# Optimization experiments

Measured on AMD Instinct MI355X. Metric: run time of the kernel, lower is better.

The kernel has to match this reference:

```python
import jax, jax.numpy as jnp
import numpy as np

HIDDEN = 32

def setup_inputs() -> dict:
    key = jax.random.key(0)
    ks = jax.random.split(key, 7)
    B, T = 131072, 128
    return {
        "x": jax.random.normal(ks[0], (B, T, 1), dtype=jnp.float32),
        "W_ih": jax.random.normal(ks[1], (4 * HIDDEN, 1), dtype=jnp.float32) * 0.1,
        "W_hh": jax.random.normal(ks[2], (4 * HIDDEN, HIDDEN), dtype=jnp.float32) * 0.1,
        "b_ih": jax.random.normal(ks[3], (4 * HIDDEN,), dtype=jnp.float32) * 0.1,
        "b_hh": jax.random.normal(ks[4], (4 * HIDDEN,), dtype=jnp.float32) * 0.1,
        "W_fc": jax.random.normal(ks[5], (2, HIDDEN), dtype=jnp.float32) * 0.1,
        "b_fc": jax.random.normal(ks[6], (2,), dtype=jnp.float32) * 0.1,
    }

def _lstm_scan(x, W_ih, W_hh, b_ih, b_hh):
    B = x.shape[0]
    h0 = jnp.zeros((B, HIDDEN), dtype=x.dtype)
    c0 = jnp.zeros((B, HIDDEN), dtype=x.dtype)
    xs = jnp.swapaxes(x, 0, 1)  # [T, B, 1]

    def step(carry, xt):
        h, c = carry
        # gates: [B, 4H]; PyTorch LSTMCell gate order: i, f, g, o
        gates = xt @ W_ih.T + b_ih + h @ W_hh.T + b_hh
        i, f, g, o = jnp.split(gates, 4, axis=-1)
        c_new = jax.nn.sigmoid(f) * c + jax.nn.sigmoid(i) * jnp.tanh(g)
        h_new = jax.nn.sigmoid(o) * jnp.tanh(c_new)
        return (h_new, c_new), None

    (h, _), _ = jax.lax.scan(step, (h0, c0), xs)
    return h

def reference(x, W_ih, W_hh, b_ih, b_hh, W_fc, b_fc):
    h = _lstm_scan(x, W_ih, W_hh, b_ih, b_hh)
    return h @ W_fc.T + b_fc  # [B, 2]
```

## Files before the change

### kernel.cpp

```cpp
#include <hip/hip_runtime.h>
#include <hip/hip_bf16.h>

#define T_STEPS 128
#define L2E  1.44269504f
#define L2E2 2.88539008f

typedef __attribute__((ext_vector_type(8))) short short8;
typedef __attribute__((ext_vector_type(4))) float f32x4;

extern "C" __global__ void __launch_bounds__(256)
lstm_mfma_kernel(const float* __restrict__ x,
                 const float* __restrict__ W_ih,
                 const float* __restrict__ W_hh,
                 const float* __restrict__ b_ih,
                 const float* __restrict__ b_hh,
                 const float* __restrict__ W_fc,
                 const float* __restrict__ b_fc,
                 float* __restrict__ out, int B)
{
    __shared__ unsigned int hhi[4][256];
    __shared__ unsigned int hlo[4][256];

    const int widx = threadIdx.x >> 6;
    const int lane = threadIdx.x & 63;
    const int p    = lane & 15;
    const int g4   = lane >> 4;
    const int btile = (blockIdx.x * 4 + widx) * 16;
    if (btile >= B) return;

    unsigned int* hh = &hhi[widx][0];
    unsigned int* hl = &hlo[widx][0];

    #pragma unroll
    for (int q = 0; q < 4; ++q) { hh[q * 64 + lane] = 0u; hl[q * 64 + lane] = 0u; }

    short8 wfrag[8];
    float  biasv[8], wihv[8];
    #pragma unroll
    for (int m = 0; m < 8; ++m) {
        int gu = (m >> 1) * 32 + 2 * p + (m & 1);
        float scale = (m >> 1) == 2 ? L2E2 : L2E;
        biasv[m] = (b_ih[gu] + b_hh[gu]) * scale;
        wihv[m]  = W_ih[gu] * scale;
        const float* wr = W_hh + gu * 32 + g4 * 8;
        short8 w;
        #pragma unroll
        for (int e = 0; e < 8; ++e) {
            unsigned int bits = __float_as_uint(wr[e] * scale);
            bits = bits + 0x7FFFu + ((bits >> 16) & 1u);
            w[e] = (short)(bits >> 16);
        }
        wfrag[m] = w;
    }

    __builtin_amdgcn_wave_barrier();

    const float* xrow = x + (size_t)(btile + g4 * 4) * T_STEPS;

    float cst[2][4];
    float hn[2][4];
    #pragma unroll
    for (int u = 0; u < 2; ++u)
        #pragma unroll
        for (int r = 0; r < 4; ++r) cst[u][r] = 0.0f;

    for (int tb = 0; tb < T_STEPS; tb += 4) {
        f32x4 xq[4];
        #pragma unroll
        for (int r = 0; r < 4; ++r)
            xq[r] = *reinterpret_cast<const f32x4*>(xrow + r * T_STEPS + tb);

        #pragma unroll
        for (int s = 0; s < 4; ++s) {
            f32x4 acc[8];
            #pragma unroll
            for (int m = 0; m < 8; ++m) {
                f32x4 a;
                #pragma unroll
                for (int r = 0; r < 4; ++r) a[r] = fmaf(xq[r][s], wihv[m], biasv[m]);
                acc[m] = a;
            }

            short8 ahi = *reinterpret_cast<short8*>(&hh[p * 16 + g4 * 4]);
            short8 alo = *reinterpret_cast<short8*>(&hl[p * 16 + g4 * 4]);

            #pragma unroll
            for (int m = 0; m < 8; ++m) {
                acc[m] = __builtin_amdgcn_mfma_f32_16x16x32_bf16(ahi, wfrag[m], acc[m], 0, 0, 0);
                acc[m] = __builtin_amdgcn_mfma_f32_16x16x32_bf16(alo, wfrag[m], acc[m], 0, 0, 0);
            }

            #pragma unroll
            for (int u = 0; u < 2; ++u) {
                #pragma unroll
                for (int r = 0; r < 4; ++r) {
                    float ei = __builtin_amdgcn_exp2f(acc[0 + u][r]);
                    float ef = __builtin_amdgcn_exp2f(acc[2 + u][r]);
                    float eg = __builtin_amdgcn_exp2f(acc[4 + u][r]);
                    float eo = __builtin_amdgcn_exp2f(acc[6 + u][r]);
                    float ef1 = ef + 1.0f, ei1 = ei + 1.0f, eg1 = eg + 1.0f;
                    float P   = ei1 * eg1;
                    float num = fmaf(ef * cst[u][r], P, ei * (eg - 1.0f) * ef1);
                    float cn  = num * __builtin_amdgcn_rcpf(P * ef1);
                    cst[u][r] = cn;
                    float ec  = __builtin_amdgcn_exp2f(cn * L2E2);
                    hn[u][r]  = eo * (ec - 1.0f)
                              * __builtin_amdgcn_rcpf((eo + 1.0f) * (ec + 1.0f));
                }
            }

            #pragma unroll
            for (int r = 0; r < 4; ++r) {
                unsigned int x0 = __float_as_uint(hn[0][r]);
                unsigned int x1 = __float_as_uint(hn[1][r]);
                unsigned int hiw = (x0 >> 16) | (x1 & 0xFFFF0000u);
                float res0 = hn[0][r] - __uint_as_float(x0 & 0xFFFF0000u);
                float res1 = hn[1][r] - __uint_as_float(x1 & 0xFFFF0000u);
                unsigned int low = (__float_as_uint(res0) >> 16)
                                 | (__float_as_uint(res1) & 0xFFFF0000u);
                int rb = g4 * 4 + r;
                hh[rb * 16 + p] = hiw;
                hl[rb * 16 + p] = low;
            }
            __builtin_amdgcn_wave_barrier();
        }
    }

    float wfc00 = W_fc[2 * p], wfc01 = W_fc[2 * p + 1];
    float wfc10 = W_fc[32 + 2 * p], wfc11 = W_fc[32 + 2 * p + 1];
    float bfc0 = b_fc[0], bfc1 = b_fc[1];
    #pragma unroll
    for (int r = 0; r < 4; ++r) {
        float o0 = fmaf(hn[0][r], wfc00, hn[1][r] * wfc01);
        float o1 = fmaf(hn[0][r], wfc10, hn[1][r] * wfc11);
        #pragma unroll
        for (int m = 8; m >= 1; m >>= 1) {
            o0 += __shfl_xor(o0, m, 64);
            o1 += __shfl_xor(o1, m, 64);
        }
        if (p == 0) {
            size_t b = (size_t)(btile + g4 * 4 + r);
            out[b * 2 + 0] = o0 + bfc0;
            out[b * 2 + 1] = o1 + bfc1;
        }
    }
}

extern "C" void kernel_launch(void* const* d_in, const int* in_sizes, int n_in,
                              void* d_out, int out_size, void* d_ws, size_t ws_size,
                              hipStream_t stream) {
    const float* x    = (const float*)d_in[0];
    const float* W_ih = (const float*)d_in[1];
    const float* W_hh = (const float*)d_in[2];
    const float* b_ih = (const float*)d_in[3];
    const float* b_hh = (const float*)d_in[4];
    const float* W_fc = (const float*)d_in[5];
    const float* b_fc = (const float*)d_in[6];
    float* out = (float*)d_out;

    int B = in_sizes[0] / T_STEPS;
    int grid = (B + 63) / 64;
    hipLaunchKernelGGL(lstm_mfma_kernel, dim3(grid), dim3(256), 0, stream,
                       x, W_ih, W_hh, b_ih, b_hh, W_fc, b_fc, out, B);
}
```

Before: 747.5 us.

## Batch reciprocals across lanes, swizzle LDS layout, and pack h with v_perm

Vectorizes the per-step LSTM cell math over f32x4 and replaces per-element reciprocals with shared ones. One rcp now serves four cell denominators and one rcp serves each pair of h denominators, using product tricks, which cuts transcendental instructions per step. The LDS write and read addresses are swizzled (pp permutation, rows written as 4*R+g4) to change the bank pattern, and bf16 hi/lo packing now uses v_perm. Batching the reciprocals adds multiplies and risks overflow or precision loss when the products of denominators grow large.

```diff
diff --git a/kernel.cpp b/kernel.cpp
--- a/kernel.cpp
+++ b/kernel.cpp
@@ -57,12 +57,12 @@
 
     const float* xrow = x + (size_t)(btile + g4 * 4) * T_STEPS;
 
-    float cst[2][4];
-    float hn[2][4];
-    #pragma unroll
-    for (int u = 0; u < 2; ++u)
-        #pragma unroll
-        for (int r = 0; r < 4; ++r) cst[u][r] = 0.0f;
+    const int pp = ((p & 3) << 2) | (p >> 2);
+    const int rdoff = pp * 16 + g4 * 4;
+
+    f32x4 cst4[2];
+    f32x4 hn4[2];
+    cst4[0] = 0.0f; cst4[1] = 0.0f;
 
     for (int tb = 0; tb < T_STEPS; tb += 4) {
         f32x4 xq[4];
@@ -72,17 +72,16 @@
 
         #pragma unroll
         for (int s = 0; s < 4; ++s) {
+            f32x4 xs;
+            xs[0] = xq[0][s]; xs[1] = xq[1][s]; xs[2] = xq[2][s]; xs[3] = xq[3][s];
+
             f32x4 acc[8];
             #pragma unroll
-            for (int m = 0; m < 8; ++m) {
-                f32x4 a;
-                #pragma unroll
-                for (int r = 0; r < 4; ++r) a[r] = fmaf(xq[r][s], wihv[m], biasv[m]);
-                acc[m] = a;
-            }
-
-            short8 ahi = *reinterpret_cast<short8*>(&hh[p * 16 + g4 * 4]);
-            short8 alo = *reinterpret_cast<short8*>(&hl[p * 16 + g4 * 4]);
+            for (int m = 0; m < 8; ++m)
+                acc[m] = xs * wihv[m] + biasv[m];
+
+            short8 ahi = *reinterpret_cast<short8*>(&hh[rdoff]);
+            short8 alo = *reinterpret_cast<short8*>(&hl[rdoff]);
 
             #pragma unroll
             for (int m = 0; m < 8; ++m) {
@@ -90,38 +89,87 @@
                 acc[m] = __builtin_amdgcn_mfma_f32_16x16x32_bf16(alo, wfrag[m], acc[m], 0, 0, 0);
             }
 
-            #pragma unroll
-            for (int u = 0; u < 2; ++u) {
-                #pragma unroll
-                for (int r = 0; r < 4; ++r) {
-                    float ei = __builtin_amdgcn_exp2f(acc[0 + u][r]);
-                    float ef = __builtin_amdgcn_exp2f(acc[2 + u][r]);
-                    float eg = __builtin_amdgcn_exp2f(acc[4 + u][r]);
-                    float eo = __builtin_amdgcn_exp2f(acc[6 + u][r]);
-                    float ef1 = ef + 1.0f, ei1 = ei + 1.0f, eg1 = eg + 1.0f;
-                    float P   = ei1 * eg1;
-                    float num = fmaf(ef * cst[u][r], P, ei * (eg - 1.0f) * ef1);
-                    float cn  = num * __builtin_amdgcn_rcpf(P * ef1);
-                    cst[u][r] = cn;
-                    float ec  = __builtin_amdgcn_exp2f(cn * L2E2);
-                    hn[u][r]  = eo * (ec - 1.0f)
-                              * __builtin_amdgcn_rcpf((eo + 1.0f) * (ec + 1.0f));
-                }
-            }
-
-            #pragma unroll
-            for (int r = 0; r < 4; ++r) {
-                unsigned int x0 = __float_as_uint(hn[0][r]);
-                unsigned int x1 = __float_as_uint(hn[1][r]);
-                unsigned int hiw = (x0 >> 16) | (x1 & 0xFFFF0000u);
-                float res0 = hn[0][r] - __uint_as_float(x0 & 0xFFFF0000u);
-                float res1 = hn[1][r] - __uint_as_float(x1 & 0xFFFF0000u);
-                unsigned int low = (__float_as_uint(res0) >> 16)
-                                 | (__float_as_uint(res1) & 0xFFFF0000u);
-                int rb = g4 * 4 + r;
-                hh[rb * 16 + p] = hiw;
-                hl[rb * 16 + p] = low;
-            }
+            #define CELL4(U) {                                                  \
+                f32x4 gi = acc[0 + (U)];                                        \
+                f32x4 gf = acc[2 + (U)];                                        \
+                f32x4 gg = acc[4 + (U)];                                        \
+                f32x4 go = acc[6 + (U)];                                        \
+                f32x4 ei, ef, eg, eo;                                           \
+                ei[0] = __builtin_amdgcn_exp2f(gi[0]);                          \
+                ei[1] = __builtin_amdgcn_exp2f(gi[1]);                          \
+                ei[2] = __builtin_amdgcn_exp2f(gi[2]);                          \
+                ei[3] = __builtin_amdgcn_exp2f(gi[3]);                          \
+                ef[0] = __builtin_amdgcn_exp2f(gf[0]);                          \
+                ef[1] = __builtin_amdgcn_exp2f(gf[1]);                          \
+                ef[2] = __builtin_amdgcn_exp2f(gf[2]);                          \
+                ef[3] = __builtin_amdgcn_exp2f(gf[3]);                          \
+                eg[0] = __builtin_amdgcn_exp2f(gg[0]);                          \
+                eg[1] = __builtin_amdgcn_exp2f(gg[1]);                          \
+                eg[2] = __builtin_amdgcn_exp2f(gg[2]);                          \
+                eg[3] = __builtin_amdgcn_exp2f(gg[3]);                          \
+                eo[0] = __builtin_amdgcn_exp2f(go[0]);                          \
+                eo[1] = __builtin_amdgcn_exp2f(go[1]);                          \
+                eo[2] = __builtin_amdgcn_exp2f(go[2]);                          \
+                eo[3] = __builtin_amdgcn_exp2f(go[3]);                          \
+                f32x4 ef1 = ef + 1.0f, ei1 = ei + 1.0f, eg1 = eg + 1.0f;        \
+                f32x4 P    = ei1 * eg1;                                         \
+                f32x4 denc = P * ef1;                                           \
+                f32x4 num  = (ef * cst4[U]) * P + (ei * (eg - 1.0f)) * ef1;     \
+                                 \
+                float d01 = denc[0] * denc[1];                                  \
+                float d23 = denc[2] * denc[3];                                  \
+                float rcq = __builtin_amdgcn_rcpf(d01 * d23);                   \
+                float r01 = d23 * rcq, r23 = d01 * rcq;                         \
+                f32x4 rc4;                                                      \
+                rc4[0] = denc[1] * r01; rc4[1] = denc[0] * r01;                 \
+                rc4[2] = denc[3] * r23; rc4[3] = denc[2] * r23;                 \
+                f32x4 cn = num * rc4;                                           \
+                cst4[U] = cn;                                                   \
+                f32x4 ec;                                                       \
+                ec[0] = __builtin_amdgcn_exp2f(cn[0] * L2E2);                   \
+                ec[1] = __builtin_amdgcn_exp2f(cn[1] * L2E2);                   \
+                ec[2] = __builtin_amdgcn_exp2f(cn[2] * L2E2);                   \
+                ec[3] = __builtin_amdgcn_exp2f(cn[3] * L2E2);                   \
+                f32x4 denh = (eo + 1.0f) * (ec + 1.0f);                         \
+                f32x4 numh = eo * (ec - 1.0f);                                  \
+                 \
+                float rh0 = __builtin_amdgcn_rcpf(denh[0] * denh[1]);           \
+                float rh1 = __builtin_amdgcn_rcpf(denh[2] * denh[3]);           \
+                f32x4 rh4;                                                      \
+                rh4[0] = denh[1] * rh0; rh4[1] = denh[0] * rh0;                 \
+                rh4[2] = denh[3] * rh1; rh4[3] = denh[2] * rh1;                 \
+                hn4[U] = numh * rh4; }
+            CELL4(0)
+            CELL4(1)
+            #undef CELL4
+
+            f32x4 tr0, tr1;
+            tr0[0] = __uint_as_float(__float_as_uint(hn4[0][0]) & 0xFFFF0000u);
+            tr0[1] = __uint_as_float(__float_as_uint(hn4[0][1]) & 0xFFFF0000u);
+            tr0[2] = __uint_as_float(__float_as_uint(hn4[0][2]) & 0xFFFF0000u);
+            tr0[3] = __uint_as_float(__float_as_uint(hn4[0][3]) & 0xFFFF0000u);
+            tr1[0] = __uint_as_float(__float_as_uint(hn4[1][0]) & 0xFFFF0000u);
+            tr1[1] = __uint_as_float(__float_as_uint(hn4[1][1]) & 0xFFFF0000u);
+            tr1[2] = __uint_as_float(__float_as_uint(hn4[1][2]) & 0xFFFF0000u);
+            tr1[3] = __uint_as_float(__float_as_uint(hn4[1][3]) & 0xFFFF0000u);
+            f32x4 res0 = hn4[0] - tr0;
+            f32x4 res1 = hn4[1] - tr1;
+
+            #define PACKR(R) {                                                  \
+                unsigned int hiw = __builtin_amdgcn_perm(                       \
+                    __float_as_uint(hn4[1][R]), __float_as_uint(hn4[0][R]),     \
+                    0x07060302u);                                               \
+                unsigned int low = __builtin_amdgcn_perm(                       \
+                    __float_as_uint(res1[R]), __float_as_uint(res0[R]),         \
+                    0x07060302u);                                               \
+                int wa = (4 * (R) + g4) * 16 + p;                               \
+                hh[wa] = hiw;                                                   \
+                hl[wa] = low; }
+            PACKR(0)
+            PACKR(1)
+            PACKR(2)
+            PACKR(3)
+            #undef PACKR
             __builtin_amdgcn_wave_barrier();
         }
     }
@@ -129,21 +177,26 @@
     float wfc00 = W_fc[2 * p], wfc01 = W_fc[2 * p + 1];
     float wfc10 = W_fc[32 + 2 * p], wfc11 = W_fc[32 + 2 * p + 1];
     float bfc0 = b_fc[0], bfc1 = b_fc[1];
-    #pragma unroll
-    for (int r = 0; r < 4; ++r) {
-        float o0 = fmaf(hn[0][r], wfc00, hn[1][r] * wfc01);
-        float o1 = fmaf(hn[0][r], wfc10, hn[1][r] * wfc11);
-        #pragma unroll
-        for (int m = 8; m >= 1; m >>= 1) {
-            o0 += __shfl_xor(o0, m, 64);
-            o1 += __shfl_xor(o1, m, 64);
-        }
-        if (p == 0) {
-            size_t b = (size_t)(btile + g4 * 4 + r);
-            out[b * 2 + 0] = o0 + bfc0;
-            out[b * 2 + 1] = o1 + bfc1;
-        }
-    }
+    #define FCR(R) {                                                            \
+        float h0 = hn4[0][R];                                                   \
+        float h1 = hn4[1][R];                                                   \
+        float o0 = fmaf(h0, wfc00, h1 * wfc01);                                 \
+        float o1 = fmaf(h0, wfc10, h1 * wfc11);                                 \
+        _Pragma("unroll")                                                       \
+        for (int mm = 8; mm >= 1; mm >>= 1) {                                   \
+            o0 += __shfl_xor(o0, mm, 64);                                       \
+            o1 += __shfl_xor(o1, mm, 64);                                       \
+        }                                                                       \
+        if (p == 0) {                                                           \
+            size_t b = (size_t)(btile + g4 * 4 + (R));                          \
+            out[b * 2 + 0] = o0 + bfc0;                                         \
+            out[b * 2 + 1] = o1 + bfc1;                                         \
+        } }
+    FCR(0)
+    FCR(1)
+    FCR(2)
+    FCR(3)
+    #undef FCR
 }
 
 extern "C" void kernel_launch(void* const* d_in, const int* in_sizes, int n_in,
```

New measurement: 736.2 us. No clear change (-1.5%).
